# Kernel tuning notes

Measured on AMD Instinct MI355X. Metric: run time of the kernel, lower is better.

## Reference

```python
import jax, jax.numpy as jnp
import numpy as np

L, H, Z, B, SRC, K = 2, 1024, 256, 128, 64, 48
IN = Z + 1 + H  # z_i (+) k (+) attn


def _init(key, shape, fan_in):
    return jax.random.normal(key, shape, jnp.float32) / np.sqrt(fan_in)


def setup_inputs() -> dict:
    key = jax.random.key(0)
    ks = jax.random.split(key, 24)
    inp = {
        "h0": jax.random.normal(ks[0], (L, B, H), jnp.float32),
        "c0": jax.random.normal(ks[1], (L, B, H), jnp.float32),
        "context": jax.random.normal(ks[2], (B, SRC, H), jnp.float32),
        "z_0": jax.random.normal(ks[3], (B, Z), jnp.float32),
        "k": jax.random.randint(ks[4], (B, 1), 1, K + 1, jnp.int32),
        "eps": jax.random.normal(ks[5], (K, B, Z), jnp.float32),
        # StackedLSTM layer 0 (input IN) and layer 1 (input H)
        "W_ih0": _init(ks[6], (4 * H, IN), IN), "W_hh0": _init(ks[7], (4 * H, H), H),
        "b_ih0": jnp.zeros((4 * H,), jnp.float32), "b_hh0": jnp.zeros((4 * H,), jnp.float32),
        "W_ih1": _init(ks[8], (4 * H, H), H), "W_hh1": _init(ks[9], (4 * H, H), H),
        "b_ih1": jnp.zeros((4 * H,), jnp.float32), "b_hh1": jnp.zeros((4 * H,), jnp.float32),
        # GlobalAttentionLatent (Luong general)
        "attn_W_in": _init(ks[10], (H, H), H), "attn_W_out": _init(ks[11], (H, 2 * H), 2 * H),
        # GeneratorLatent
        "mu_W": _init(ks[12], (Z, H), H), "mu_b": jnp.zeros((Z,), jnp.float32),
        "sigma_W": _init(ks[13], (Z, H), H), "sigma_b": jnp.zeros((Z,), jnp.float32),
    }
    return inp


def _lstm_cell(x, h, c, W_ih, W_hh, b_ih, b_hh):
    gates = x @ W_ih.T + b_ih + h @ W_hh.T + b_hh
    i, f, g, o = jnp.split(gates, 4, axis=1)
    c_new = jax.nn.sigmoid(f) * c + jax.nn.sigmoid(i) * jnp.tanh(g)
    h_new = jax.nn.sigmoid(o) * jnp.tanh(c_new)
    return h_new, c_new


def _attend(q, context, W_in, W_out):
    # q: [B,H], context: [B,S,H] -> [B,H]
    scores = jnp.einsum('bsh,bh->bs', context, q @ W_in.T)
    align = jax.nn.softmax(scores, axis=1)
    weighted = jnp.einsum('bs,bsh->bh', align, context)
    return jnp.tanh(jnp.concatenate([weighted, q], axis=1) @ W_out.T)


def _forward(h0, c0, context, z_0, k, eps,
             W_ih0, W_hh0, b_ih0, b_hh0, W_ih1, W_hh1, b_ih1, b_hh1,
             attn_W_in, attn_W_out, mu_W, mu_b, sigma_W, sigma_b):
    k_max = eps.shape[0]
    k_f = k.astype(jnp.float32)  # [B,1]
    attn0 = _attend(c0[-1], context, attn_W_in, attn_W_out)

    def step(carry, inp):
        z_i, attn_o, h, c = carry
        i, eps_i = inp
        x = jnp.concatenate([z_i, k_f, attn_o], axis=1)  # [B, Z+1+H]
        h0n, c0n = _lstm_cell(x, h[0], c[0], W_ih0, W_hh0, b_ih0, b_hh0)
        h1n, c1n = _lstm_cell(h0n, h[1], c[1], W_ih1, W_hh1, b_ih1, b_hh1)
        h_new = jnp.stack([h0n, h1n])
        c_new = jnp.stack([c0n, c1n])
        frozen = (i >= k_f).astype(h_new.dtype)[None]  # [1,B,1]
        h_new = frozen * h + (1.0 - frozen) * h_new
        c_new = frozen * c + (1.0 - frozen) * c_new
        output = h1n  # rnn output before freezing, as in torch
        mu_i = output @ mu_W.T + mu_b
        sig_i = output @ sigma_W.T + sigma_b
        z_next = mu_i + jnp.exp(sig_i) * eps_i
        attn_new = _attend(output, context, attn_W_in, attn_W_out)
        return (z_next, attn_new, h_new, c_new), (z_next, mu_i, sig_i)

    steps = jnp.arange(k_max, dtype=jnp.float32)
    (_, _, h_f, c_f), (z, mu, sigma) = jax.lax.scan(
        step, (z_0, attn0, h0, c0), (steps, eps))
    valid = (steps[:, None] < k_f[:, 0][None, :])[:, :, None]  # [K,B,1]
    z = jnp.where(valid, z, 0.0)
    mu = jnp.where(valid, mu, 0.0)
    sigma = jnp.where(valid, sigma, 0.0)
    return (z.transpose(1, 0, 2), mu.transpose(1, 0, 2), sigma.transpose(1, 0, 2), h_f, c_f)


def reference(h0, c0, context, z_0, k, eps,
              W_ih0, W_hh0, b_ih0, b_hh0, W_ih1, W_hh1, b_ih1, b_hh1,
              attn_W_in, attn_W_out, mu_W, mu_b, sigma_W, sigma_b):
    return _forward(h0, c0, context, z_0, k, eps,
                    W_ih0, W_hh0, b_ih0, b_hh0, W_ih1, W_hh1, b_ih1, b_hh1,
                    attn_W_in, attn_W_out, mu_W, mu_b, sigma_W, sigma_b)
```

## Files before the change

kernel.cpp:

```cpp
#include <hip/hip_runtime.h>
#include <hip/hip_bf16.h>

#define L_ 2
#define H_ 1024
#define Z_ 256
#define B_ 128
#define SRC_ 64
#define K_ 48
#define BH_ (B_ * H_)
#define BZ_ (B_ * Z_)
#define BKZ_ ((size_t)B_ * K_ * Z_)
#define KA_ 2304
#define KB_ 2048

typedef unsigned short u16;
typedef __attribute__((ext_vector_type(8))) short short8;
typedef __attribute__((ext_vector_type(4))) float f32x4;

__device__ __align__(16) u16 g_Wc0[4096 * KA_];
__device__ __align__(16) u16 g_Wc1[4096 * KB_];
__device__ __align__(16) u16 g_Wmq[512 * 1024];
__device__ __align__(16) u16 g_Woutb[1024 * 2048];
__device__ __align__(16) u16 g_WinT[1024 * 1024];
__device__ __align__(16) u16 g_ctxb[8192 * 1024];
__device__ __align__(16) u16 g_ctxW[8192 * 1024];
__device__ __align__(16) u16 g_ctxWin[8192 * 1024];
__device__ __align__(16) u16 g_XA[2][B_ * KA_];
__device__ __align__(16) u16 g_XB[2][B_ * KB_];
__device__ __align__(16) u16 g_XC[B_ * H_];
__device__ float g_pb0[4096], g_pb1[4096], g_pbmq[512], g_wk0[4096];
__device__ float g_cs0[BH_], g_cs1[BH_], g_align[B_ * SRC_];
__device__ float g_cred[B_ * H_];
__device__ int g_perm[B_], g_inv[B_], g_kr[B_], g_Mact[K_];

__device__ __forceinline__ float sigm(float x) { return 1.0f / (1.0f + expf(-x)); }
__device__ __forceinline__ u16 f2b(float f) {
    union { float f; unsigned u; } x; x.f = f;
    unsigned r = x.u + 0x7fffu + ((x.u >> 16) & 1u);
    return (u16)(r >> 16);
}
__device__ __forceinline__ float b2f(u16 s) {
    union { unsigned u; float f; } x; x.u = ((unsigned)s) << 16;
    return x.f;
}

__global__ void k_sort(const int* __restrict__ kvec) {
    __shared__ int ks[B_];
    int t = threadIdx.x;
    if (t < B_) ks[t] = kvec[t];
    __syncthreads();
    if (t < B_) {
        int kb = ks[t], rank = 0;
        for (int j = 0; j < B_; ++j) { int kj = ks[j]; rank += (kj > kb) || (kj == kb && j < t); }
        g_perm[rank] = t; g_inv[t] = rank; g_kr[rank] = kb;
    }
    if (t < K_) { int c = 0; for (int j = 0; j < B_; ++j) c += (ks[j] > t); g_Mact[t] = c; }
}

__global__ void k_zero(float* __restrict__ out) {
    size_t n = 3 * BKZ_;
    for (size_t i = (size_t)blockIdx.x * 256 + threadIdx.x; i < n; i += (size_t)gridDim.x * 256)
        out[i] = 0.f;
}

__global__ void prep_wc0(const float* __restrict__ Wih, const float* __restrict__ Whh,
                         const float* __restrict__ bih, const float* __restrict__ bhh) {
    int n = blockIdx.x;
    int h = n >> 2, g = n & 3, r = g * 1024 + h;
    u16* row = g_Wc0 + (size_t)n * KA_;
    for (int j = threadIdx.x; j < KA_; j += 256) {
        float v = (j < 256) ? Wih[(size_t)r * 1281 + j]
                : (j < 1280) ? Wih[(size_t)r * 1281 + j + 1]
                             : Whh[(size_t)r * 1024 + (j - 1280)];
        row[j] = f2b(v);
    }
    if (threadIdx.x == 0) {
        g_wk0[n] = Wih[(size_t)r * 1281 + 256];
        g_pb0[n] = bih[r] + bhh[r];
    }
}

__global__ void prep_wc1(const float* __restrict__ Wih, const float* __restrict__ Whh,
                         const float* __restrict__ bih, const float* __restrict__ bhh) {
    int n = blockIdx.x;
    int h = n >> 2, g = n & 3, r = g * 1024 + h;
    u16* row = g_Wc1 + (size_t)n * KB_;
    for (int j = threadIdx.x; j < KB_; j += 256) {
        float v = (j < 1024) ? Wih[(size_t)r * 1024 + j] : Whh[(size_t)r * 1024 + (j - 1024)];
        row[j] = f2b(v);
    }
    if (threadIdx.x == 0) g_pb1[n] = bih[r] + bhh[r];
}

__global__ void prep_wmq(const float* __restrict__ muW, const float* __restrict__ mub,
                         const float* __restrict__ sgW, const float* __restrict__ sgb) {
    int n = blockIdx.x;
    int z = n >> 1, sel = n & 1;
    const float* src = sel ? sgW : muW;
    u16* row = g_Wmq + (size_t)n * 1024;
    for (int j = threadIdx.x; j < 1024; j += 256) row[j] = f2b(src[(size_t)z * 1024 + j]);
    if (threadIdx.x == 0) g_pbmq[n] = sel ? sgb[z] : mub[z];
}

__global__ void prep_copy(const float* __restrict__ in, u16* __restrict__ out, int n) {
    for (int i = blockIdx.x * 256 + threadIdx.x; i < n; i += gridDim.x * 256)
        out[i] = f2b(in[i]);
}

__global__ void prep_winT(const float* __restrict__ Win) {
    __shared__ float t[32][33];
    int bx = blockIdx.x * 32, by = blockIdx.y * 32;
    int tx = threadIdx.x & 31, ty0 = threadIdx.x >> 5;
    for (int it = 0; it < 4; ++it) {
        int ty = ty0 + it * 8;
        t[ty][tx] = Win[(size_t)(by + ty) * 1024 + bx + tx];
    }
    __syncthreads();
    for (int it = 0; it < 4; ++it) {
        int ty = ty0 + it * 8;
        g_WinT[(size_t)(bx + ty) * 1024 + by + tx] = f2b(t[tx][ty]);
    }
}

template <int K>
__device__ __forceinline__ void mmq(const u16* __restrict__ A, int sA,
                                    const u16* __restrict__ W, int sW,
                                    int m0, int n0, int w, int lane, f32x4& acc) {
    constexpr int KQ = K / 4;
    const int quad = lane >> 4, l16 = lane & 15;
    const u16* pa = A + (size_t)(m0 + l16) * sA + w * KQ + quad * 8;
    const u16* pw = W + (size_t)(n0 + l16) * sW + w * KQ + quad * 8;
#pragma unroll 4
    for (int k0 = 0; k0 < KQ; k0 += 32) {
        short8 a = *(const short8*)(const void*)(pa + k0);
        short8 b = *(const short8*)(const void*)(pw + k0);
        acc = __builtin_amdgcn_mfma_f32_16x16x32_bf16(a, b, acc, 0, 0, 0);
    }
}

__device__ __forceinline__ void stage_q(float* sm, int w, int lane, const f32x4& acc) {
    int quad = lane >> 4, l16 = lane & 15;
#pragma unroll
    for (int r = 0; r < 4; ++r) sm[w * 272 + (quad * 4 + r) * 17 + l16] = acc[r];
}

template <int K>
__device__ __forceinline__ void mm32(const u16* __restrict__ A, int sA,
                                     const u16* __restrict__ W, int sW,
                                     int m0, int n0, int w, int lane, f32x4 acc[2][2]) {
    constexpr int KQ = K / 4;
    const int quad = lane >> 4, l16 = lane & 15;
    const u16* pa0 = A + (size_t)(m0 + l16) * sA + w * KQ + quad * 8;
    const u16* pa1 = pa0 + (size_t)16 * sA;
    const u16* pb0 = W + (size_t)(n0 + l16) * sW + w * KQ + quad * 8;
    const u16* pb1 = pb0 + (size_t)16 * sW;
#pragma unroll 2
    for (int k0 = 0; k0 < KQ; k0 += 32) {
        short8 a0 = *(const short8*)(const void*)(pa0 + k0);
        short8 a1 = *(const short8*)(const void*)(pa1 + k0);
        short8 b0 = *(const short8*)(const void*)(pb0 + k0);
        short8 b1 = *(const short8*)(const void*)(pb1 + k0);
        acc[0][0] = __builtin_amdgcn_mfma_f32_16x16x32_bf16(a0, b0, acc[0][0], 0, 0, 0);
        acc[0][1] = __builtin_amdgcn_mfma_f32_16x16x32_bf16(a0, b1, acc[0][1], 0, 0, 0);
        acc[1][0] = __builtin_amdgcn_mfma_f32_16x16x32_bf16(a1, b0, acc[1][0], 0, 0, 0);
        acc[1][1] = __builtin_amdgcn_mfma_f32_16x16x32_bf16(a1, b1, acc[1][1], 0, 0, 0);
    }
}

template <int LAYER>
__global__ __launch_bounds__(256) void k_lstm(int step) {
    constexpr int K = (LAYER == 0) ? KA_ : KB_;
    const int p = step & 1;
    const u16* A = (LAYER == 0) ? g_XA[p] : g_XB[p];
    const u16* W = (LAYER == 0) ? g_Wc0 : g_Wc1;
    const float* pb = (LAYER == 0) ? g_pb0 : g_pb1;
    float* cs = (LAYER == 0) ? g_cs0 : g_cs1;
    const u16* stOld = (LAYER == 0) ? (g_XA[p] + 1280) : (g_XB[p] + 1024);
    u16* stNew = (LAYER == 0) ? (g_XA[1 - p] + 1280) : (g_XB[1 - p] + 1024);
    u16* hout = (LAYER == 0) ? g_XB[p] : g_XC;
    const int hoStride = (LAYER == 0) ? KB_ : 1024;

    const int tid = threadIdx.x, w = tid >> 6, lane = tid & 63;
    const int xcd = blockIdx.x & 7, loc = blockIdx.x >> 3;
    const int mt = loc & 3, nl = loc >> 2;
    const int m0 = mt * 32;
    const int n0 = (xcd * 16 + nl) * 32;
    const int Mact = g_Mact[step];

    if (m0 >= Mact) {
        const int r = m0 + (tid & 31), hg = (n0 >> 2) + (tid >> 5);
        stNew[(size_t)r * K + hg] = stOld[(size_t)r * K + hg];
        return;
    }

    __shared__ float smf[4 * 32 * 33];
    f32x4 acc[2][2] = {};
    mm32<K>(A, K, W, K, m0, n0, w, lane, acc);
    const int quad = lane >> 4, l16 = lane & 15;
#pragma unroll
    for (int i = 0; i < 2; ++i)
#pragma unroll
        for (int j = 0; j < 2; ++j)
#pragma unroll
            for (int r = 0; r < 4; ++r)
                smf[(w * 32 + i * 16 + quad * 4 + r) * 33 + j * 16 + l16] = acc[i][j][r];
    __syncthreads();
    const int bl = tid & 31, hl = tid >> 5;
    const int r = m0 + bl;
    float g[4];
#pragma unroll
    for (int gg = 0; gg < 4; ++gg) {
        int c = hl * 4 + gg;
        float s = smf[bl * 33 + c] + smf[(32 + bl) * 33 + c] +
                  smf[(64 + bl) * 33 + c] + smf[(96 + bl) * 33 + c];
        g[gg] = s + pb[n0 + c];
    }
    const int kr = g_kr[r];
    if (LAYER == 0) {
        float kf = (float)kr;
#pragma unroll
        for (int gg = 0; gg < 4; ++gg) g[gg] += kf * g_wk0[n0 + hl * 4 + gg];
    }
    const int hg = (n0 >> 2) + hl;
    float cold = cs[r * 1024 + hg];
    float cn = sigm(g[1]) * cold + sigm(g[0]) * tanhf(g[2]);
    float hn = sigm(g[3]) * tanhf(cn);
    hout[(size_t)r * hoStride + hg] = f2b(hn);
    if (step < kr) {
        stNew[(size_t)r * K + hg] = f2b(hn);
        cs[r * 1024 + hg] = cn;
    } else {
        stNew[(size_t)r * K + hg] = stOld[(size_t)r * K + hg];
    }
}

__global__ __launch_bounds__(256) void k_mix(const float* __restrict__ eps,
                                             float* __restrict__ out, int step,
                                             int do_mu, int do_sc) {
    __shared__ float sm[1344];
    const int tid = threadIdx.x;
    const int Mact = g_Mact[step];
    if (blockIdx.x < 256) {
        if (!do_mu) return;
        const int w = tid >> 6, lane = tid & 63;
        const int xcd = blockIdx.x & 7, loc = blockIdx.x >> 3;
        const int mt = loc & 7, nl = loc >> 3;
        const int m0 = mt * 16;
        const int n0 = (xcd * 4 + nl) * 16;
        if (m0 >= Mact) return;
        f32x4 acc = {0.f, 0.f, 0.f, 0.f};
        mmq<1024>(g_XC, 1024, g_Wmq, 1024, m0, n0, w, lane, acc);
        stage_q(sm, w, lane, acc);
        __syncthreads();
        if (tid < 128) {
            int bl = tid & 15, zl = tid >> 4;
            int r = m0 + bl;
            int c0 = 2 * zl, c1 = 2 * zl + 1;
            float mu = sm[bl * 17 + c0] + sm[272 + bl * 17 + c0] +
                       sm[544 + bl * 17 + c0] + sm[816 + bl * 17 + c0] + g_pbmq[n0 + c0];
            float sg = sm[bl * 17 + c1] + sm[272 + bl * 17 + c1] +
                       sm[544 + bl * 17 + c1] + sm[816 + bl * 17 + c1] + g_pbmq[n0 + c1];
            int zg = (n0 >> 1) + zl;
            int b = g_perm[r];
            float e = eps[((size_t)step * B_ + b) * Z_ + zg];
            float zn = mu + expf(sg) * e;
            g_XA[(step + 1) & 1][(size_t)r * KA_ + zg] = f2b(zn);
            bool valid = step < g_kr[r];
            size_t o = ((size_t)b * K_ + step) * Z_ + zg;
            out[o] = valid ? zn : 0.f;
            out[BKZ_ + o] = valid ? mu : 0.f;
            out[2 * BKZ_ + o] = valid ? sg : 0.f;
        }
    } else if (blockIdx.x < 384) {
        if (!do_sc) return;
        const int r = blockIdx.x - 256;
        if (r >= Mact) return;
        float* qf = sm;
        float* parts = sm + 1024;
        for (int i = tid; i < 1024; i += 256) qf[i] = b2f(g_XC[r * 1024 + i]);
        __syncthreads();
        int s = tid >> 2, part = tid & 3;
        const int b = g_perm[r];
        const u16* row = g_ctxWin + ((size_t)(b * SRC_ + s)) * 1024 + part * 256;
        float pacc = 0.f;
        for (int j = 0; j < 256; j += 8) {
            short8 v = *(const short8*)(const void*)(row + j);
#pragma unroll
            for (int t = 0; t < 8; ++t) pacc += qf[part * 256 + j + t] * b2f(((u16*)&v)[t]);
        }
        parts[s * 4 + part] = pacc;
        __syncthreads();
        if (tid < 64) {
            float v = parts[tid * 4] + parts[tid * 4 + 1] + parts[tid * 4 + 2] + parts[tid * 4 + 3];
            float mx = v;
            for (int o = 32; o; o >>= 1) mx = fmaxf(mx, __shfl_xor(mx, o, 64));
            float e = expf(v - mx), sum = e;
            for (int o = 32; o; o >>= 1) sum += __shfl_xor(sum, o, 64);
            g_align[r * SRC_ + tid] = e / sum;
        }
    } else {
        if (!do_sc) return;
        const int w = tid >> 6, lane = tid & 63;
        const int t = blockIdx.x - 384;
        const int xcd = t & 7, loc = t >> 3;
        const int mt = loc & 7, nl = loc >> 3;
        const int m0 = mt * 16;
        const int n0 = (xcd * 8 + nl) * 16;
        if (m0 >= Mact) return;
        f32x4 acc = {0.f, 0.f, 0.f, 0.f};
        mmq<1024>(g_XC, 1024, g_Woutb + 1024, 2048, m0, n0, w, lane, acc);
        stage_q(sm, w, lane, acc);
        __syncthreads();
        int bl = tid >> 4, hc = tid & 15;
        float cred = sm[bl * 17 + hc] + sm[272 + bl * 17 + hc] +
                     sm[544 + bl * 17 + hc] + sm[816 + bl * 17 + hc];
        g_cred[(size_t)(m0 + bl) * 1024 + n0 + hc] = cred;
    }
}

__global__ __launch_bounds__(256) void k_contract(int dp, int step) {
    __shared__ float sm[16 * SRC_];
    const int tid = threadIdx.x;
    const int xcd = blockIdx.x & 7, loc = blockIdx.x >> 3;
    const int mt = loc & 7, nl = loc >> 3;
    const int m0 = mt * 16;
    const int n0 = (xcd * 8 + nl) * 16;
    if (m0 >= g_Mact[step]) return;
    for (int i = tid; i < 16 * SRC_; i += 256)
        sm[i] = g_align[(m0 + (i >> 6)) * SRC_ + (i & 63)];
    __syncthreads();
    int bl = tid >> 4, hc = tid & 15;
    int r = m0 + bl;
    const int b = g_perm[r];
    const u16* base = g_ctxW + ((size_t)b * SRC_) * 1024 + n0 + hc;
    float a = g_cred[(size_t)r * 1024 + n0 + hc];
#pragma unroll 8
    for (int s = 0; s < SRC_; ++s) a += sm[bl * 64 + s] * b2f(base[(size_t)s * 1024]);
    g_XA[dp][(size_t)r * KA_ + 256 + n0 + hc] = f2b(tanhf(a));
}

__global__ void k_init(const float* __restrict__ h0, const float* __restrict__ c0,
                       const float* __restrict__ z0) {
    int i = blockIdx.x * 256 + threadIdx.x;
    int b = i >> 10, h = i & 1023;
    int r = g_inv[b];
    g_XA[0][(size_t)r * KA_ + 1280 + h] = f2b(h0[i]);
    g_XB[0][(size_t)r * KB_ + 1024 + h] = f2b(h0[BH_ + i]);
    g_XC[r * 1024 + h] = f2b(c0[BH_ + i]);
    g_cs0[r * 1024 + h] = c0[i];
    g_cs1[r * 1024 + h] = c0[BH_ + i];
    if (i < BZ_) {
        int bb = i >> 8, z = i & 255;
        g_XA[0][(size_t)g_inv[bb] * KA_ + z] = f2b(z0[i]);
    }
}

__global__ void k_final(float* __restrict__ out) {
    int i = blockIdx.x * 256 + threadIdx.x;
    int b = i >> 10, h = i & 1023;
    int r = g_inv[b];
    float* hf = out + (size_t)3 * BKZ_;
    float* cf = hf + 2 * BH_;
    hf[i] = b2f(g_XA[0][(size_t)r * KA_ + 1280 + h]);
    hf[BH_ + i] = b2f(g_XB[0][(size_t)r * KB_ + 1024 + h]);
    cf[i] = g_cs0[r * 1024 + h];
    cf[BH_ + i] = g_cs1[r * 1024 + h];
}

__global__ __launch_bounds__(256) void k_gemm_prep(const u16* __restrict__ A, int sA,
                                                   const u16* __restrict__ W, int sW,
                                                   u16* __restrict__ Out, int sO) {
    const int tid = threadIdx.x, w = tid >> 6, lane = tid & 63;
    const int quad = lane >> 4, l16 = lane & 15;
    const int xcd = blockIdx.x & 7, loc = blockIdx.x >> 3;
    const int n0 = (xcd * 2 + (loc & 1)) * 64;
    const int mb = (loc >> 1) * 128 + w * 32;
    f32x4 acc[2][4] = {};
    const u16* pa0 = A + (size_t)(mb + l16) * sA + quad * 8;
    const u16* pa1 = pa0 + (size_t)16 * sA;
    const u16* pw = W + (size_t)(n0 + l16) * sW + quad * 8;
#pragma unroll 2
    for (int k0 = 0; k0 < 1024; k0 += 32) {
        short8 a0 = *(const short8*)(const void*)(pa0 + k0);
        short8 a1 = *(const short8*)(const void*)(pa1 + k0);
#pragma unroll
        for (int j = 0; j < 4; ++j) {
            short8 b = *(const short8*)(const void*)(pw + (size_t)j * 16 * sW + k0);
            acc[0][j] = __builtin_amdgcn_mfma_f32_16x16x32_bf16(a0, b, acc[0][j], 0, 0, 0);
            acc[1][j] = __builtin_amdgcn_mfma_f32_16x16x32_bf16(a1, b, acc[1][j], 0, 0, 0);
        }
    }
#pragma unroll
    for (int i = 0; i < 2; ++i)
#pragma unroll
        for (int j = 0; j < 4; ++j)
#pragma unroll
            for (int r = 0; r < 4; ++r)
                Out[(size_t)(mb + i * 16 + quad * 4 + r) * sO + n0 + j * 16 + l16] =
                    f2b(acc[i][j][r]);
}

extern "C" void kernel_launch(void* const* d_in, const int* in_sizes, int n_in,
                              void* d_out, int out_size, void* d_ws, size_t ws_size,
                              hipStream_t stream) {
    (void)in_sizes; (void)n_in; (void)out_size; (void)d_ws; (void)ws_size;
    const float* h0 = (const float*)d_in[0];
    const float* c0 = (const float*)d_in[1];
    const float* ctx = (const float*)d_in[2];
    const float* z0 = (const float*)d_in[3];
    const int* kvec = (const int*)d_in[4];
    const float* eps = (const float*)d_in[5];
    const float* Wih0 = (const float*)d_in[6];
    const float* Whh0 = (const float*)d_in[7];
    const float* bih0 = (const float*)d_in[8];
    const float* bhh0 = (const float*)d_in[9];
    const float* Wih1 = (const float*)d_in[10];
    const float* Whh1 = (const float*)d_in[11];
    const float* bih1 = (const float*)d_in[12];
    const float* bhh1 = (const float*)d_in[13];
    const float* Win = (const float*)d_in[14];
    const float* Wout = (const float*)d_in[15];
    const float* muW = (const float*)d_in[16];
    const float* mub = (const float*)d_in[17];
    const float* sgW = (const float*)d_in[18];
    const float* sgb = (const float*)d_in[19];
    float* out = (float*)d_out;

    dim3 blk(256);
    k_sort<<<1, 128, 0, stream>>>(kvec);
    k_zero<<<2048, blk, 0, stream>>>(out);
    prep_wc0<<<4096, blk, 0, stream>>>(Wih0, Whh0, bih0, bhh0);
    prep_wc1<<<4096, blk, 0, stream>>>(Wih1, Whh1, bih1, bhh1);
    prep_wmq<<<512, blk, 0, stream>>>(muW, mub, sgW, sgb);
    {
        u16* woutb; hipGetSymbolAddress((void**)&woutb, HIP_SYMBOL(g_Woutb));
        u16* ctxb; hipGetSymbolAddress((void**)&ctxb, HIP_SYMBOL(g_ctxb));
        u16* winT; hipGetSymbolAddress((void**)&winT, HIP_SYMBOL(g_WinT));
        u16* ctxW; hipGetSymbolAddress((void**)&ctxW, HIP_SYMBOL(g_ctxW));
        u16* ctxWin; hipGetSymbolAddress((void**)&ctxWin, HIP_SYMBOL(g_ctxWin));
        prep_copy<<<2048, blk, 0, stream>>>(Wout, woutb, 1024 * 2048);
        prep_copy<<<8192, blk, 0, stream>>>(ctx, ctxb, 8192 * 1024);
        prep_winT<<<dim3(32, 32), blk, 0, stream>>>(Win);
        k_gemm_prep<<<1024, blk, 0, stream>>>(ctxb, 1024, woutb, 2048, ctxW, 1024);
        k_gemm_prep<<<1024, blk, 0, stream>>>(ctxb, 1024, winT, 1024, ctxWin, 1024);
    }
    k_init<<<BH_ / 256, blk, 0, stream>>>(h0, c0, z0);
    k_mix<<<896, blk, 0, stream>>>(eps, out, 0, 0, 1);
    k_contract<<<512, blk, 0, stream>>>(0, 0);

    for (int i = 0; i < K_; ++i) {
        k_lstm<0><<<512, blk, 0, stream>>>(i);
        k_lstm<1><<<512, blk, 0, stream>>>(i);
        const int more = (i + 1 < K_) ? 1 : 0;
        k_mix<<<896, blk, 0, stream>>>(eps, out, i, 1, more);
        if (more) k_contract<<<512, blk, 0, stream>>>((i + 1) & 1, i);
    }
    k_final<<<BH_ / 256, blk, 0, stream>>>(out);
}
```

Before: 3.213 ms.

## Fuse attention scores, softmax, output projection and context contraction into one kernel

Merges the attention-score/softmax blocks, the W_out query GEMM and the separate k_contract kernel into one k_mix2 kernel. Each block now recomputes scores and softmax for its 8 rows in shared memory, then runs the MFMA projection and the context contraction. This removes one launch per step and the g_align/g_cred global round trips. In exchange the score dot products are computed redundantly across the column tiles. It also merges the two prep GEMMs into one launch and raises the LSTM inner-loop unroll.

Result: slower. 5.435 ms (+69.2%).

```diff
diff --git a/kernel.cpp b/kernel.cpp
--- a/kernel.cpp
+++ b/kernel.cpp
@@ -29,8 +29,7 @@
 __device__ __align__(16) u16 g_XB[2][B_ * KB_];
 __device__ __align__(16) u16 g_XC[B_ * H_];
 __device__ float g_pb0[4096], g_pb1[4096], g_pbmq[512], g_wk0[4096];
-__device__ float g_cs0[BH_], g_cs1[BH_], g_align[B_ * SRC_];
-__device__ float g_cred[B_ * H_];
+__device__ float g_cs0[BH_], g_cs1[BH_];
 __device__ int g_perm[B_], g_inv[B_], g_kr[B_], g_Mact[K_];
 
 __device__ __forceinline__ float sigm(float x) { return 1.0f / (1.0f + expf(-x)); }
@@ -154,7 +153,7 @@
     const u16* pa1 = pa0 + (size_t)16 * sA;
     const u16* pb0 = W + (size_t)(n0 + l16) * sW + w * KQ + quad * 8;
     const u16* pb1 = pb0 + (size_t)16 * sW;
-#pragma unroll 2
+#pragma unroll 4
     for (int k0 = 0; k0 < KQ; k0 += 32) {
         short8 a0 = *(const short8*)(const void*)(pa0 + k0);
         short8 a1 = *(const short8*)(const void*)(pa1 + k0);
@@ -234,9 +233,9 @@
     }
 }
 
-__global__ __launch_bounds__(256) void k_mix(const float* __restrict__ eps,
-                                             float* __restrict__ out, int step,
-                                             int do_mu, int do_sc) {
+__global__ __launch_bounds__(256) void k_mix2(const float* __restrict__ eps,
+                                              float* __restrict__ out, int step, int dp,
+                                              int do_mu, int do_sc) {
     __shared__ float sm[1344];
     const int tid = threadIdx.x;
     const int Mact = g_Mact[step];
@@ -264,79 +263,87 @@
             int b = g_perm[r];
             float e = eps[((size_t)step * B_ + b) * Z_ + zg];
             float zn = mu + expf(sg) * e;
-            g_XA[(step + 1) & 1][(size_t)r * KA_ + zg] = f2b(zn);
+            g_XA[dp][(size_t)r * KA_ + zg] = f2b(zn);
             bool valid = step < g_kr[r];
             size_t o = ((size_t)b * K_ + step) * Z_ + zg;
             out[o] = valid ? zn : 0.f;
             out[BKZ_ + o] = valid ? mu : 0.f;
             out[2 * BKZ_ + o] = valid ? sg : 0.f;
         }
-    } else if (blockIdx.x < 384) {
-        if (!do_sc) return;
-        const int r = blockIdx.x - 256;
-        if (r >= Mact) return;
-        float* qf = sm;
-        float* parts = sm + 1024;
-        for (int i = tid; i < 1024; i += 256) qf[i] = b2f(g_XC[r * 1024 + i]);
-        __syncthreads();
-        int s = tid >> 2, part = tid & 3;
-        const int b = g_perm[r];
-        const u16* row = g_ctxWin + ((size_t)(b * SRC_ + s)) * 1024 + part * 256;
-        float pacc = 0.f;
-        for (int j = 0; j < 256; j += 8) {
-            short8 v = *(const short8*)(const void*)(row + j);
-#pragma unroll
-            for (int t = 0; t < 8; ++t) pacc += qf[part * 256 + j + t] * b2f(((u16*)&v)[t]);
-        }
-        parts[s * 4 + part] = pacc;
-        __syncthreads();
-        if (tid < 64) {
-            float v = parts[tid * 4] + parts[tid * 4 + 1] + parts[tid * 4 + 2] + parts[tid * 4 + 3];
-            float mx = v;
-            for (int o = 32; o; o >>= 1) mx = fmaxf(mx, __shfl_xor(mx, o, 64));
-            float e = expf(v - mx), sum = e;
-            for (int o = 32; o; o >>= 1) sum += __shfl_xor(sum, o, 64);
-            g_align[r * SRC_ + tid] = e / sum;
-        }
     } else {
         if (!do_sc) return;
+        const int idx = blockIdx.x - 256;
+        const int m16 = idx & 7;
+        const int half = (idx >> 3) & 1;
+        const int j = idx >> 4;
+        const int m0 = m16 * 16;
+        if (m0 >= Mact) return;
+        const int r0 = m0 + half * 8;
+        const int n0 = j * 128;
+        const int row8 = tid >> 5, t32 = tid & 31;
+        {
+            const int r = r0 + row8;
+            const int b = g_perm[r];
+            const u16* q = g_XC + (size_t)r * 1024;
+            const u16* cp = g_ctxWin + ((size_t)(b * SRC_ + t32)) * 1024;
+            float d0 = 0.f, d1 = 0.f;
+            for (int h = 0; h < 1024; h += 8) {
+                short8 qv = *(const short8*)(const void*)(q + h);
+                short8 v0 = *(const short8*)(const void*)(cp + h);
+                short8 v1 = *(const short8*)(const void*)(cp + 32 * 1024 + h);
+#pragma unroll
+                for (int e = 0; e < 8; ++e) {
+                    float qe = b2f(((const u16*)&qv)[e]);
+                    d0 += qe * b2f(((const u16*)&v0)[e]);
+                    d1 += qe * b2f(((const u16*)&v1)[e]);
+                }
+            }
+            float mx = fmaxf(d0, d1);
+            for (int o = 16; o; o >>= 1) mx = fmaxf(mx, __shfl_xor(mx, o, 32));
+            float e0 = expf(d0 - mx), e1 = expf(d1 - mx);
+            float sum = e0 + e1;
+            for (int o = 16; o; o >>= 1) sum += __shfl_xor(sum, o, 32);
+            float inv = 1.f / sum;
+            sm[row8 * 64 + t32] = e0 * inv;
+            sm[row8 * 64 + t32 + 32] = e1 * inv;
+        }
+        __syncthreads();
         const int w = tid >> 6, lane = tid & 63;
-        const int t = blockIdx.x - 384;
-        const int xcd = t & 7, loc = t >> 3;
-        const int mt = loc & 7, nl = loc >> 3;
-        const int m0 = mt * 16;
-        const int n0 = (xcd * 8 + nl) * 16;
-        if (m0 >= Mact) return;
-        f32x4 acc = {0.f, 0.f, 0.f, 0.f};
-        mmq<1024>(g_XC, 1024, g_Woutb + 1024, 2048, m0, n0, w, lane, acc);
-        stage_q(sm, w, lane, acc);
-        __syncthreads();
-        int bl = tid >> 4, hc = tid & 15;
-        float cred = sm[bl * 17 + hc] + sm[272 + bl * 17 + hc] +
-                     sm[544 + bl * 17 + hc] + sm[816 + bl * 17 + hc];
-        g_cred[(size_t)(m0 + bl) * 1024 + n0 + hc] = cred;
-    }
-}
-
-__global__ __launch_bounds__(256) void k_contract(int dp, int step) {
-    __shared__ float sm[16 * SRC_];
-    const int tid = threadIdx.x;
-    const int xcd = blockIdx.x & 7, loc = blockIdx.x >> 3;
-    const int mt = loc & 7, nl = loc >> 3;
-    const int m0 = mt * 16;
-    const int n0 = (xcd * 8 + nl) * 16;
-    if (m0 >= g_Mact[step]) return;
-    for (int i = tid; i < 16 * SRC_; i += 256)
-        sm[i] = g_align[(m0 + (i >> 6)) * SRC_ + (i & 63)];
-    __syncthreads();
-    int bl = tid >> 4, hc = tid & 15;
-    int r = m0 + bl;
-    const int b = g_perm[r];
-    const u16* base = g_ctxW + ((size_t)b * SRC_) * 1024 + n0 + hc;
-    float a = g_cred[(size_t)r * 1024 + n0 + hc];
+        const int quad = lane >> 4, l16 = lane & 15;
+        const int wn0 = n0 + w * 32;
+        const u16* pa = g_XC + (size_t)(m0 + l16) * 1024 + quad * 8;
+        const u16* pw0 = g_Woutb + 1024 + (size_t)(wn0 + l16) * 2048 + quad * 8;
+        const u16* pw1 = pw0 + (size_t)16 * 2048;
+        f32x4 ca = {0.f, 0.f, 0.f, 0.f}, cb = {0.f, 0.f, 0.f, 0.f};
+#pragma unroll 4
+        for (int k0 = 0; k0 < 1024; k0 += 32) {
+            short8 av = *(const short8*)(const void*)(pa + k0);
+            short8 b0 = *(const short8*)(const void*)(pw0 + k0);
+            short8 b1 = *(const short8*)(const void*)(pw1 + k0);
+            ca = __builtin_amdgcn_mfma_f32_16x16x32_bf16(av, b0, ca, 0, 0, 0);
+            cb = __builtin_amdgcn_mfma_f32_16x16x32_bf16(av, b1, cb, 0, 0, 0);
+        }
+        if ((quad >> 1) == half) {
+#pragma unroll
+            for (int sub = 0; sub < 2; ++sub) {
+                const int c = wn0 + sub * 16 + l16;
+                const f32x4& cc = sub ? cb : ca;
+#pragma unroll
+                for (int reg = 0; reg < 4; ++reg) {
+                    const int lrow = quad * 4 + reg;
+                    const int lr = lrow - half * 8;
+                    const int rr = m0 + lrow;
+                    const int b2 = g_perm[rr];
+                    const u16* base = g_ctxW + ((size_t)b2 * SRC_) * 1024 + c;
+                    float a = cc[reg];
 #pragma unroll 8
-    for (int s = 0; s < SRC_; ++s) a += sm[bl * 64 + s] * b2f(base[(size_t)s * 1024]);
-    g_XA[dp][(size_t)r * KA_ + 256 + n0 + hc] = f2b(tanhf(a));
+                    for (int s = 0; s < SRC_; ++s)
+                        a += sm[lr * 64 + s] * b2f(base[(size_t)s * 1024]);
+                    g_XA[dp][(size_t)rr * KA_ + 256 + c] = f2b(tanhf(a));
+                }
+            }
+        }
+    }
 }
 
 __global__ void k_init(const float* __restrict__ h0, const float* __restrict__ c0,
@@ -367,17 +374,20 @@
     cf[BH_ + i] = g_cs1[r * 1024 + h];
 }
 
-__global__ __launch_bounds__(256) void k_gemm_prep(const u16* __restrict__ A, int sA,
-                                                   const u16* __restrict__ W, int sW,
-                                                   u16* __restrict__ Out, int sO) {
+__global__ __launch_bounds__(256) void k_prep3() {
     const int tid = threadIdx.x, w = tid >> 6, lane = tid & 63;
     const int quad = lane >> 4, l16 = lane & 15;
     const int xcd = blockIdx.x & 7, loc = blockIdx.x >> 3;
-    const int n0 = (xcd * 2 + (loc & 1)) * 64;
-    const int mb = (loc >> 1) * 128 + w * 32;
+    const int mt8 = loc & 7, job = loc >> 3;
+    const int sel = job >> 4, nt = job & 15;
+    const u16* W = sel ? g_WinT : g_Woutb;
+    const int sW = sel ? 1024 : 2048;
+    u16* Out = sel ? g_ctxWin : g_ctxW;
+    const int n0 = nt * 64;
+    const int mb = (xcd * 8 + mt8) * 128 + w * 32;
     f32x4 acc[2][4] = {};
-    const u16* pa0 = A + (size_t)(mb + l16) * sA + quad * 8;
-    const u16* pa1 = pa0 + (size_t)16 * sA;
+    const u16* pa0 = g_ctxb + (size_t)(mb + l16) * 1024 + quad * 8;
+    const u16* pa1 = pa0 + (size_t)16 * 1024;
     const u16* pw = W + (size_t)(n0 + l16) * sW + quad * 8;
 #pragma unroll 2
     for (int k0 = 0; k0 < 1024; k0 += 32) {
@@ -396,7 +406,7 @@
         for (int j = 0; j < 4; ++j)
 #pragma unroll
             for (int r = 0; r < 4; ++r)
-                Out[(size_t)(mb + i * 16 + quad * 4 + r) * sO + n0 + j * 16 + l16] =
+                Out[(size_t)(mb + i * 16 + quad * 4 + r) * 1024 + n0 + j * 16 + l16] =
                     f2b(acc[i][j][r]);
 }
 
@@ -435,25 +445,19 @@
     {
         u16* woutb; hipGetSymbolAddress((void**)&woutb, HIP_SYMBOL(g_Woutb));
         u16* ctxb; hipGetSymbolAddress((void**)&ctxb, HIP_SYMBOL(g_ctxb));
-        u16* winT; hipGetSymbolAddress((void**)&winT, HIP_SYMBOL(g_WinT));
-        u16* ctxW; hipGetSymbolAddress((void**)&ctxW, HIP_SYMBOL(g_ctxW));
-        u16* ctxWin; hipGetSymbolAddress((void**)&ctxWin, HIP_SYMBOL(g_ctxWin));
         prep_copy<<<2048, blk, 0, stream>>>(Wout, woutb, 1024 * 2048);
         prep_copy<<<8192, blk, 0, stream>>>(ctx, ctxb, 8192 * 1024);
         prep_winT<<<dim3(32, 32), blk, 0, stream>>>(Win);
-        k_gemm_prep<<<1024, blk, 0, stream>>>(ctxb, 1024, woutb, 2048, ctxW, 1024);
-        k_gemm_prep<<<1024, blk, 0, stream>>>(ctxb, 1024, winT, 1024, ctxWin, 1024);
+        k_prep3<<<2048, blk, 0, stream>>>();
     }
     k_init<<<BH_ / 256, blk, 0, stream>>>(h0, c0, z0);
-    k_mix<<<896, blk, 0, stream>>>(eps, out, 0, 0, 1);
-    k_contract<<<512, blk, 0, stream>>>(0, 0);
+    k_mix2<<<384, blk, 0, stream>>>(eps, out, 0, 0, 0, 1);
 
     for (int i = 0; i < K_; ++i) {
         k_lstm<0><<<512, blk, 0, stream>>>(i);
         k_lstm<1><<<512, blk, 0, stream>>>(i);
         const int more = (i + 1 < K_) ? 1 : 0;
-        k_mix<<<896, blk, 0, stream>>>(eps, out, i, 1, more);
-        if (more) k_contract<<<512, blk, 0, stream>>>((i + 1) & 1, i);
+        k_mix2<<<384, blk, 0, stream>>>(eps, out, i, (i + 1) & 1, 1, more);
     }
     k_final<<<BH_ / 256, blk, 0, stream>>>(out);
 }
```
